# Optimization experiments

Hardware: AMD Instinct MI355X
Metric: run time of the kernel (lower is better)

Reference implementation:

```python
import jax, jax.numpy as jnp
import numpy as np

N = 100000   # nodes
E = 800000   # directed edges (before self loops)
D = 300      # feature dim (SGConv(300, 300))


def setup_inputs() -> dict:
    key = jax.random.key(0)
    k1, k2, k3, k4 = jax.random.split(key, 4)
    x = jax.random.normal(k1, (N, D), dtype=jnp.float32)
    edge_index = jax.random.randint(k2, (2, E), 0, N, dtype=jnp.int32)
    # Linear(300, 300) params (kaiming-uniform-ish scale)
    bound = 1.0 / np.sqrt(D)
    W = jax.random.uniform(k3, (D, D), jnp.float32, -bound, bound)
    b = jax.random.uniform(k4, (D,), jnp.float32, -bound, bound)
    return {"x": x, "edge_index": edge_index, "W": W, "b": b}


def _sgc_forward(x, edge_index, W, b):
    n = x.shape[0]
    # --- GCN normalization with self loops (PyG SGConv defaults, K=1) ---
    loop = jnp.arange(n, dtype=edge_index.dtype)
    row = jnp.concatenate([edge_index[0], loop])   # source nodes
    col = jnp.concatenate([edge_index[1], loop])   # target nodes (aggregation index)
    deg = jax.ops.segment_sum(jnp.ones_like(col, dtype=x.dtype), col, num_segments=n)
    dinv = jnp.where(deg > 0, jax.lax.rsqrt(deg), 0.0)
    w = dinv[row] * dinv[col]                      # [E+N] edge norm
    # --- one hop of sparse propagation: out[c] += w * x[r] ---
    h = jax.ops.segment_sum(x[row] * w[:, None], col, num_segments=n)  # [N, D]
    # --- linear map ---
    h = h @ W.T + b
    # --- relu (dropout p=0 is identity) ---
    h = jax.nn.relu(h)
    # --- F.normalize: row-wise L2 with eps clamp ---
    norm = jnp.linalg.norm(h, axis=-1, keepdims=True)
    return h / jnp.maximum(norm, 1e-12)


def reference(x, edge_index, W, b):
    return _sgc_forward(x, edge_index, W, b)
```

## Files before the change

kernel.cpp:

```cpp
#include <hip/hip_runtime.h>
#include <hip/hip_bf16.h>
#include <stdint.h>

#define D 300
#define KP 320
#define JP 304
#define NT 19

typedef __hip_bfloat16 bf16;
typedef __bf16 bf16x8 __attribute__((ext_vector_type(8)));
typedef unsigned short us8 __attribute__((ext_vector_type(8)));
typedef float f32x4 __attribute__((ext_vector_type(4)));

static __device__ __forceinline__ unsigned short f2bu(float f) {
    bf16 h = __float2bfloat16(f);
    return *reinterpret_cast<unsigned short*>(&h);
}
static __device__ __forceinline__ float bulo(unsigned int u) {
    return __uint_as_float(u << 16);
}
static __device__ __forceinline__ float buhi(unsigned int u) {
    return __uint_as_float(u & 0xffff0000u);
}
static __device__ __forceinline__ void gload_lds16(const void* g, void* l) {
    __builtin_amdgcn_global_load_lds(
        (const __attribute__((address_space(1))) unsigned int*)g,
        (__attribute__((address_space(3))) unsigned int*)l, 16, 0, 0);
}

__global__ void k_count_twb(const int* __restrict__ col, int* __restrict__ deg, int e,
                            const float* __restrict__ W, unsigned short* __restrict__ wbp,
                            int cb) {
    int bid = blockIdx.x;
    if (bid < cb) {
        int i = bid * 256 + threadIdx.x;
        if (i < e) atomicAdd(&deg[col[i]], 1);
    } else {
        int idx = (bid - cb) * 256 + threadIdx.x;
        if (idx < JP * KP) {
            int i = idx & 7;
            int lrow = (idx >> 3) & 15;
            int kg = (idx >> 7) & 3;
            int q = idx >> 9;
            int kk = q / 19, t = q - kk * 19;
            int j = t * 16 + lrow;
            int k = kk * 32 + kg * 8 + i;
            wbp[idx] = (j < D && k < D) ? f2bu(W[j * D + k]) : (unsigned short)0;
        }
    }
}

__global__ void k_scanA(const int* __restrict__ deg, int* __restrict__ ex,
                        float* __restrict__ dinv, int* __restrict__ bsum, int n) {
    __shared__ int sh[256];
    int tid = threadIdx.x;
    int base = blockIdx.x * 1024 + tid * 4;
    int v[4]; int s = 0;
#pragma unroll
    for (int t = 0; t < 4; t++) {
        int i = base + t;
        v[t] = (i < n) ? deg[i] : 0;
        if (i < n) dinv[i] = rsqrtf((float)(v[t] + 1));
        s += v[t];
    }
    sh[tid] = s;
    __syncthreads();
    for (int off = 1; off < 256; off <<= 1) {
        int t = (tid >= off) ? sh[tid - off] : 0;
        __syncthreads();
        sh[tid] += t;
        __syncthreads();
    }
    int excl = sh[tid] - s;
#pragma unroll
    for (int t = 0; t < 4; t++) {
        int i = base + t;
        if (i < n) ex[i] = excl;
        excl += v[t];
    }
    if (tid == 255) bsum[blockIdx.x] = sh[255];
}

__global__ void k_scanB(const int* __restrict__ bsum, int* __restrict__ bexc, int nb) {
    __shared__ int sh[256];
    int tid = threadIdx.x;
    int s = (tid < nb) ? bsum[tid] : 0;
    sh[tid] = s;
    __syncthreads();
    for (int off = 1; off < 256; off <<= 1) {
        int t = (tid >= off) ? sh[tid - off] : 0;
        __syncthreads();
        sh[tid] += t;
        __syncthreads();
    }
    bexc[tid] = sh[tid] - s;
}

__global__ __launch_bounds__(256)
void k_zmm_fill(const float* __restrict__ x, const unsigned short* __restrict__ wbp,
                unsigned short* __restrict__ zb, int n, int zblocks,
                const int* __restrict__ ei, const float* __restrict__ dinv,
                const int* __restrict__ ex, const int* __restrict__ bexc,
                int* __restrict__ cursor, uint2* __restrict__ edges, int e) {
    __shared__ unsigned short Wsh[2][JP * 32];
    if (blockIdx.x >= zblocks) {
        int i = (int)(blockIdx.x - zblocks) * 256 + threadIdx.x;
        if (i < e) {
            int r = ei[i];
            int c = ei[e + i];
            int p = atomicAdd(&cursor[c], 1);
            edges[ex[c] + bexc[c >> 10] + p] =
                make_uint2((unsigned int)r, __float_as_uint(dinv[r] * dinv[c]));
        }
        return;
    }
    int tid = threadIdx.x;
    int lane = tid & 63, wid = tid >> 6;
    int r0 = blockIdx.x * 64 + wid * 16;
    int lrow = lane & 15, kg = lane >> 4;

    int soff[5];
#pragma unroll
    for (int j = 0; j < 5; j++) {
        int i = wid + 4 * j;
        soff[j] = (i < 19) ? (i * 1024 + lane * 16) : -1;
    }
    const char* wb = (const char*)wbp;

    int arow = r0 + lrow; if (arow >= n) arow = n - 1;
    const float* xr = x + (size_t)arow * D;

    f32x4 acc[NT];
#pragma unroll
    for (int t = 0; t < NT; t++) acc[t] = f32x4{0.f, 0.f, 0.f, 0.f};

    float4 pa, pb;
    {
        int c = kg * 8;
        pa = *(const float4*)(xr + c);
        pb = *(const float4*)(xr + c + 4);
#pragma unroll
        for (int j = 0; j < 5; j++)
            if (soff[j] >= 0) gload_lds16(wb + soff[j], (char*)&Wsh[0][0] + soff[j]);
    }
    __syncthreads();

    for (int kk = 0; kk < KP / 32; kk++) {
        float4 na, nb2;
        if (kk < KP / 32 - 1) {
            int c = (kk + 1) * 32 + kg * 8;
            int clo = (c <= 296) ? c : 0;
            int chi = (c <= 292) ? c + 4 : 0;
            na  = *(const float4*)(xr + clo);
            nb2 = *(const float4*)(xr + chi);
            int gof = (kk + 1) * (JP * 64);
            char* lbase = (char*)&Wsh[(kk + 1) & 1][0];
#pragma unroll
            for (int j = 0; j < 5; j++)
                if (soff[j] >= 0) gload_lds16(wb + gof + soff[j], lbase + soff[j]);
        }
        us8 au;
        au[0] = f2bu(pa.x); au[1] = f2bu(pa.y); au[2] = f2bu(pa.z); au[3] = f2bu(pa.w);
        au[4] = f2bu(pb.x); au[5] = f2bu(pb.y); au[6] = f2bu(pb.z); au[7] = f2bu(pb.w);
        bf16x8 av = __builtin_bit_cast(bf16x8, au);
        const unsigned short* bbase = &Wsh[kk & 1][0] + lane * 8;
#pragma unroll
        for (int t = 0; t < NT; t++) {
            bf16x8 bv = __builtin_bit_cast(bf16x8, *(const us8*)(bbase + t * 512));
            acc[t] = __builtin_amdgcn_mfma_f32_16x16x32_bf16(av, bv, acc[t], 0, 0, 0);
        }
        __syncthreads();
        pa = na; pb = nb2;
    }

#pragma unroll
    for (int r = 0; r < 4; r++) {
        int g0 = r0 + kg * 4 + r;
        if (g0 < n) {
            unsigned short* zp0 = zb + (size_t)g0 * JP;
#pragma unroll
            for (int t = 0; t < NT; t++) {
                int j = t * 16 + lrow;
                zp0[j] = f2bu(acc[t][r]);
            }
        }
    }
}

__global__ void k_zgather(const uint2* __restrict__ zb2, const uint2* __restrict__ edges,
                          const int* __restrict__ ex, const int* __restrict__ bexc,
                          const int* __restrict__ deg, const float* __restrict__ dinv,
                          const float* __restrict__ bias, float* __restrict__ out, int n) {
    int w = (blockIdx.x * blockDim.x + threadIdx.x) >> 6;
    if (w >= n) return;
    int lane = threadIdx.x & 63;
    int s = ex[w] + bexc[w >> 10];
    int cnt = deg[w];
    float dc = dinv[w];
    const bool p2 = lane < 12;
    float a0 = 0.f, a1 = 0.f, a2 = 0.f, a3 = 0.f;
    float a4 = 0.f, a5 = 0.f, a6 = 0.f, a7 = 0.f;
    const uint2 Z = make_uint2(0u, 0u);

#define GACC(ua, ub, wgt)                                                     \
    {                                                                         \
        a0 += (wgt) * bulo((ua).x); a1 += (wgt) * buhi((ua).x);               \
        a2 += (wgt) * bulo((ua).y); a3 += (wgt) * buhi((ua).y);               \
        a4 += (wgt) * bulo((ub).x); a5 += (wgt) * buhi((ub).x);               \
        a6 += (wgt) * bulo((ub).y); a7 += (wgt) * buhi((ub).y);               \
    }

    int t = 0;
    for (; t + 4 <= cnt; t += 4) {
        uint2 e0 = edges[s + t],     e1 = edges[s + t + 1];
        uint2 e2 = edges[s + t + 2], e3 = edges[s + t + 3];
        const uint2* q0 = zb2 + (size_t)e0.x * 76 + lane;
        const uint2* q1 = zb2 + (size_t)e1.x * 76 + lane;
        const uint2* q2 = zb2 + (size_t)e2.x * 76 + lane;
        const uint2* q3 = zb2 + (size_t)e3.x * 76 + lane;
        uint2 u0a = q0[0], u1a = q1[0], u2a = q2[0], u3a = q3[0];
        uint2 u0b = p2 ? q0[64] : Z;
        uint2 u1b = p2 ? q1[64] : Z;
        uint2 u2b = p2 ? q2[64] : Z;
        uint2 u3b = p2 ? q3[64] : Z;
        float w0 = __uint_as_float(e0.y), w1 = __uint_as_float(e1.y);
        float w2 = __uint_as_float(e2.y), w3 = __uint_as_float(e3.y);
        GACC(u0a, u0b, w0);
        GACC(u1a, u1b, w1);
        GACC(u2a, u2b, w2);
        GACC(u3a, u3b, w3);
    }
    for (; t < cnt; t++) {
        uint2 ed = edges[s + t];
        float wg = __uint_as_float(ed.y);
        const uint2* q = zb2 + (size_t)ed.x * 76 + lane;
        uint2 ua = q[0];
        uint2 ub = p2 ? q[64] : Z;
        GACC(ua, ub, wg);
    }
    {
        float sw = dc * dc;
        const uint2* q = zb2 + (size_t)w * 76 + lane;
        uint2 ua = q[0];
        uint2 ub = p2 ? q[64] : Z;
        GACC(ua, ub, sw);
    }
#undef GACC

    float4 b0 = *(const float4*)(bias + 4 * lane);
    float4 b1 = {0.f, 0.f, 0.f, 0.f};
    const bool wr2 = lane < 11;
    if (wr2) b1 = *(const float4*)(bias + 256 + 4 * lane);
    float v0 = fmaxf(a0 + b0.x, 0.f), v1 = fmaxf(a1 + b0.y, 0.f);
    float v2 = fmaxf(a2 + b0.z, 0.f), v3 = fmaxf(a3 + b0.w, 0.f);
    float v4 = fmaxf(a4 + b1.x, 0.f), v5 = fmaxf(a5 + b1.y, 0.f);
    float v6 = fmaxf(a6 + b1.z, 0.f), v7 = fmaxf(a7 + b1.w, 0.f);
    float sq = v0 * v0 + v1 * v1 + v2 * v2 + v3 * v3
             + v4 * v4 + v5 * v5 + v6 * v6 + v7 * v7;
    sq += __shfl_xor(sq, 1);
    sq += __shfl_xor(sq, 2);
    sq += __shfl_xor(sq, 4);
    sq += __shfl_xor(sq, 8);
    sq += __shfl_xor(sq, 16);
    sq += __shfl_xor(sq, 32);
    float sc = rsqrtf(fmaxf(sq, 1e-24f));

    float* op = out + (size_t)w * D;
    f32x4 o0 = {v0 * sc, v1 * sc, v2 * sc, v3 * sc};
    __builtin_nontemporal_store(o0, (f32x4*)(op + 4 * lane));
    if (wr2) {
        f32x4 o1 = {v4 * sc, v5 * sc, v6 * sc, v7 * sc};
        __builtin_nontemporal_store(o1, (f32x4*)(op + 256 + 4 * lane));
    }
}

extern "C" void kernel_launch(void* const* d_in, const int* in_sizes, int n_in,
                              void* d_out, int out_size, void* d_ws, size_t ws_size,
                              hipStream_t stream) {
    const float* x  = (const float*)d_in[0];
    const int*   ei = (const int*)d_in[1];
    const float* W  = (const float*)d_in[2];
    const float* b  = (const float*)d_in[3];
    float* out = (float*)d_out;
    int n = in_sizes[0] / D;
    int e = in_sizes[1] / 2;

    char* p = (char*)d_ws;
    unsigned short* zb = (unsigned short*)p; p += (size_t)n * JP * 2;
    int* deg = (int*)p;         p += (size_t)n * 4;
    int* cursor = (int*)p;      p += (size_t)n * 4;
    float* dinv = (float*)p;    p += (size_t)n * 4;
    int* ex = (int*)p;          p += (size_t)n * 4;
    p = (char*)(((uintptr_t)p + 15) & ~(uintptr_t)15);
    uint2* edges = (uint2*)p;   p += (size_t)e * 8;
    int* bsum = (int*)p;        p += 256 * 4;
    int* bexc = (int*)p;        p += 256 * 4;
    p = (char*)(((uintptr_t)p + 15) & ~(uintptr_t)15);
    unsigned short* wbp = (unsigned short*)p; p += (size_t)JP * KP * 2;

    int nb = (n + 1023) / 1024;
    int cb = (e + 255) / 256;
    int tb = (JP * KP + 255) / 256;
    int zblocks = (n + 63) / 64;
    int fb = (e + 255) / 256;

    (void)hipMemsetAsync(deg, 0, (size_t)n * 8, stream);
    k_count_twb<<<cb + tb, 256, 0, stream>>>(ei + e, deg, e, W, wbp, cb);
    k_scanA<<<nb, 256, 0, stream>>>(deg, ex, dinv, bsum, n);
    k_scanB<<<1, 256, 0, stream>>>(bsum, bexc, nb);
    k_zmm_fill<<<zblocks + fb, 256, 0, stream>>>(x, wbp, zb, n, zblocks,
                                                 ei, dinv, ex, bexc, cursor, edges, e);
    k_zgather<<<(n + 3) / 4, 256, 0, stream>>>((const uint2*)zb, edges, ex, bexc,
                                               deg, dinv, b, out, n);
}
```

Measured before the change: 222.9 us.

## Make zmm persistent with LDS-resident weights split in two column halves

```diff
diff --git a/kernel.cpp b/kernel.cpp
--- a/kernel.cpp
+++ b/kernel.cpp
@@ -5,7 +5,10 @@
 #define D 300
 #define KP 320
 #define JP 304
-#define NT 19
+#define P0_SHORTS 51200
+#define P0_BYTES  102400
+#define P1_BYTES  92160
+#define LDS_BYTES 102400
 
 typedef __hip_bfloat16 bf16;
 typedef __bf16 bf16x8 __attribute__((ext_vector_type(8)));
@@ -38,12 +41,18 @@
     } else {
         int idx = (bid - cb) * 256 + threadIdx.x;
         if (idx < JP * KP) {
-            int i = idx & 7;
-            int lrow = (idx >> 3) & 15;
-            int kg = (idx >> 7) & 3;
-            int q = idx >> 9;
-            int kk = q / 19, t = q - kk * 19;
-            int j = t * 16 + lrow;
+            int local, tbase, kk, tloc;
+            if (idx < P0_SHORTS) {
+                local = idx; tbase = 0;
+                int q = local >> 9; kk = q / 10; tloc = q - kk * 10;
+            } else {
+                local = idx - P0_SHORTS; tbase = 10;
+                int q = local >> 9; kk = q / 9; tloc = q - kk * 9;
+            }
+            int i = local & 7;
+            int lrow = (local >> 3) & 15;
+            int kg = (local >> 7) & 3;
+            int j = (tbase + tloc) * 16 + lrow;
             int k = kk * 32 + kg * 8 + i;
             wbp[idx] = (j < D && k < D) ? f2bu(W[j * D + k]) : (unsigned short)0;
         }
@@ -96,94 +105,101 @@
     bexc[tid] = sh[tid] - s;
 }
 
-__global__ __launch_bounds__(256)
+template<int NTp, int TOFF>
+static __device__ __forceinline__
+void zmm_rows(const float* __restrict__ x, const unsigned short* Wsh,
+              unsigned short* __restrict__ zb, int n, int nrt, int bid,
+              int wid, int lane) {
+    int lrow = lane & 15, kg = lane >> 4;
+    for (int rt = bid; rt < nrt; rt += 256) {
+        int r0 = rt * 64 + wid * 16;
+        int arow = r0 + lrow; if (arow >= n) arow = n - 1;
+        const float* xr = x + (size_t)arow * D;
+        f32x4 acc[NTp];
+#pragma unroll
+        for (int t = 0; t < NTp; t++) acc[t] = f32x4{0.f, 0.f, 0.f, 0.f};
+        float4 pa = *(const float4*)(xr + kg * 8);
+        float4 pb = *(const float4*)(xr + kg * 8 + 4);
+        float4 qa = *(const float4*)(xr + 32 + kg * 8);
+        float4 qb = *(const float4*)(xr + 32 + kg * 8 + 4);
+        for (int kk = 0; kk < 10; kk++) {
+            float4 ra, rb;
+            if (kk < 8) {
+                int c = (kk + 2) * 32 + kg * 8;
+                int clo = (c <= 296) ? c : 0;
+                int chi = (c <= 292) ? c + 4 : 0;
+                ra = *(const float4*)(xr + clo);
+                rb = *(const float4*)(xr + chi);
+            }
+            us8 au;
+            au[0] = f2bu(pa.x); au[1] = f2bu(pa.y); au[2] = f2bu(pa.z); au[3] = f2bu(pa.w);
+            au[4] = f2bu(pb.x); au[5] = f2bu(pb.y); au[6] = f2bu(pb.z); au[7] = f2bu(pb.w);
+            bf16x8 av = __builtin_bit_cast(bf16x8, au);
+            const unsigned short* bbase = Wsh + kk * (NTp * 512) + lane * 8;
+#pragma unroll
+            for (int t = 0; t < NTp; t++) {
+                bf16x8 bv = __builtin_bit_cast(bf16x8, *(const us8*)(bbase + t * 512));
+                acc[t] = __builtin_amdgcn_mfma_f32_16x16x32_bf16(av, bv, acc[t], 0, 0, 0);
+            }
+            pa = qa; pb = qb; qa = ra; qb = rb;
+        }
+#pragma unroll
+        for (int r = 0; r < 4; r++) {
+            int g0 = r0 + kg * 4 + r;
+            if (g0 < n) {
+                unsigned short* zp = zb + (size_t)g0 * JP + TOFF;
+#pragma unroll
+                for (int t = 0; t < NTp; t++) zp[t * 16 + lrow] = f2bu(acc[t][r]);
+            }
+        }
+    }
+}
+
+__global__ __launch_bounds__(320)
 void k_zmm_fill(const float* __restrict__ x, const unsigned short* __restrict__ wbp,
-                unsigned short* __restrict__ zb, int n, int zblocks,
+                unsigned short* __restrict__ zb, int n,
                 const int* __restrict__ ei, const float* __restrict__ dinv,
                 const int* __restrict__ ex, const int* __restrict__ bexc,
                 int* __restrict__ cursor, uint2* __restrict__ edges, int e) {
-    __shared__ unsigned short Wsh[2][JP * 32];
-    if (blockIdx.x >= zblocks) {
-        int i = (int)(blockIdx.x - zblocks) * 256 + threadIdx.x;
-        if (i < e) {
+    extern __shared__ unsigned short Wsh[];
+    int tid = threadIdx.x;
+    int bid = blockIdx.x;
+    int lane = tid & 63, wid = tid >> 6;
+    int nrt = (n + 63) >> 6;
+    const char* wb = (const char*)wbp;
+
+#pragma unroll
+    for (int j = 0; j < 20; j++) {
+        int byte = (tid + 320 * j) * 16;
+        gload_lds16(wb + byte, (char*)Wsh + byte);
+    }
+    __syncthreads();
+
+    if (wid < 4) {
+        zmm_rows<10, 0>(x, Wsh, zb, n, nrt, bid, wid, lane);
+    } else {
+        int echunk = (e + 255) >> 8;
+        int lo = bid * echunk;
+        int hi = lo + echunk; if (hi > e) hi = e;
+        for (int i = lo + lane; i < hi; i += 64) {
             int r = ei[i];
             int c = ei[e + i];
             int p = atomicAdd(&cursor[c], 1);
             edges[ex[c] + bexc[c >> 10] + p] =
                 make_uint2((unsigned int)r, __float_as_uint(dinv[r] * dinv[c]));
         }
-        return;
-    }
-    int tid = threadIdx.x;
-    int lane = tid & 63, wid = tid >> 6;
-    int r0 = blockIdx.x * 64 + wid * 16;
-    int lrow = lane & 15, kg = lane >> 4;
-
-    int soff[5];
-#pragma unroll
-    for (int j = 0; j < 5; j++) {
-        int i = wid + 4 * j;
-        soff[j] = (i < 19) ? (i * 1024 + lane * 16) : -1;
-    }
-    const char* wb = (const char*)wbp;
-
-    int arow = r0 + lrow; if (arow >= n) arow = n - 1;
-    const float* xr = x + (size_t)arow * D;
-
-    f32x4 acc[NT];
-#pragma unroll
-    for (int t = 0; t < NT; t++) acc[t] = f32x4{0.f, 0.f, 0.f, 0.f};
-
-    float4 pa, pb;
-    {
-        int c = kg * 8;
-        pa = *(const float4*)(xr + c);
-        pb = *(const float4*)(xr + c + 4);
-#pragma unroll
-        for (int j = 0; j < 5; j++)
-            if (soff[j] >= 0) gload_lds16(wb + soff[j], (char*)&Wsh[0][0] + soff[j]);
-    }
-    __syncthreads();
-
-    for (int kk = 0; kk < KP / 32; kk++) {
-        float4 na, nb2;
-        if (kk < KP / 32 - 1) {
-            int c = (kk + 1) * 32 + kg * 8;
-            int clo = (c <= 296) ? c : 0;
-            int chi = (c <= 292) ? c + 4 : 0;
-            na  = *(const float4*)(xr + clo);
-            nb2 = *(const float4*)(xr + chi);
-            int gof = (kk + 1) * (JP * 64);
-            char* lbase = (char*)&Wsh[(kk + 1) & 1][0];
-#pragma unroll
-            for (int j = 0; j < 5; j++)
-                if (soff[j] >= 0) gload_lds16(wb + gof + soff[j], lbase + soff[j]);
-        }
-        us8 au;
-        au[0] = f2bu(pa.x); au[1] = f2bu(pa.y); au[2] = f2bu(pa.z); au[3] = f2bu(pa.w);
-        au[4] = f2bu(pb.x); au[5] = f2bu(pb.y); au[6] = f2bu(pb.z); au[7] = f2bu(pb.w);
-        bf16x8 av = __builtin_bit_cast(bf16x8, au);
-        const unsigned short* bbase = &Wsh[kk & 1][0] + lane * 8;
-#pragma unroll
-        for (int t = 0; t < NT; t++) {
-            bf16x8 bv = __builtin_bit_cast(bf16x8, *(const us8*)(bbase + t * 512));
-            acc[t] = __builtin_amdgcn_mfma_f32_16x16x32_bf16(av, bv, acc[t], 0, 0, 0);
-        }
-        __syncthreads();
-        pa = na; pb = nb2;
-    }
-
-#pragma unroll
-    for (int r = 0; r < 4; r++) {
-        int g0 = r0 + kg * 4 + r;
-        if (g0 < n) {
-            unsigned short* zp0 = zb + (size_t)g0 * JP;
-#pragma unroll
-            for (int t = 0; t < NT; t++) {
-                int j = t * 16 + lrow;
-                zp0[j] = f2bu(acc[t][r]);
-            }
-        }
+    }
+    __syncthreads();
+
+#pragma unroll
+    for (int j = 0; j < 18; j++) {
+        int byte = (tid + 320 * j) * 16;
+        gload_lds16(wb + P0_BYTES + byte, (char*)Wsh + byte);
+    }
+    __syncthreads();
+
+    if (wid < 4) {
+        zmm_rows<9, 160>(x, Wsh, zb, n, nrt, bid, wid, lane);
     }
 }
 
@@ -301,15 +317,15 @@
     int nb = (n + 1023) / 1024;
     int cb = (e + 255) / 256;
     int tb = (JP * KP + 255) / 256;
-    int zblocks = (n + 63) / 64;
-    int fb = (e + 255) / 256;
 
     (void)hipMemsetAsync(deg, 0, (size_t)n * 8, stream);
     k_count_twb<<<cb + tb, 256, 0, stream>>>(ei + e, deg, e, W, wbp, cb);
     k_scanA<<<nb, 256, 0, stream>>>(deg, ex, dinv, bsum, n);
     k_scanB<<<1, 256, 0, stream>>>(bsum, bexc, nb);
-    k_zmm_fill<<<zblocks + fb, 256, 0, stream>>>(x, wbp, zb, n, zblocks,
-                                                 ei, dinv, ex, bexc, cursor, edges, e);
+    (void)hipFuncSetAttribute((const void*)k_zmm_fill,
+                              hipFuncAttributeMaxDynamicSharedMemorySize, LDS_BYTES);
+    k_zmm_fill<<<256, 320, LDS_BYTES, stream>>>(x, wbp, zb, n,
+                                                ei, dinv, ex, bexc, cursor, edges, e);
     k_zgather<<<(n + 3) / 4, 256, 0, stream>>>((const uint2*)zb, edges, ex, bexc,
                                                deg, dinv, b, out, n);
 }
```

After: 454.9 us. 104% more time.
